# Kernel optimization log

Hardware: AMD Instinct MI355X
Metric: run time of the kernel (lower is better)

## Reference

```python
import jax, jax.numpy as jnp
import numpy as np
from jax import lax

B = 32; L_HIST = 96; FUT = 96; N = 862
D_MODEL = 512; D_STATE = 16; D_CONV = 4; EXPAND = 2
D_INNER = EXPAND * D_MODEL
DT_RANK = (D_MODEL + 15) // 16  # ceil(d_model/16) = 32
D_FF = 512; E_LAYERS = 2; EPS = 1e-5


def setup_inputs() -> dict:
    key = jax.random.key(0)
    ks = iter(jax.random.split(key, 64))
    def rn(shape, scale=0.02):
        return jax.random.normal(next(ks), shape, dtype=jnp.float32) * scale
    f32 = jnp.float32
    inp = {
        "history_data": jax.random.normal(next(ks), (B, L_HIST, N, 1), dtype=f32),
        # RevIN affine
        "revin_w": jnp.ones((N,), f32), "revin_b": jnp.zeros((N,), f32),
        # inverted embedding Linear(L_hist -> d_model)
        "embed_w": rn((D_MODEL, L_HIST)), "embed_b": jnp.zeros((D_MODEL,), f32),
        # Mamba params, stacked over [e_layers, 2 directions]
        "in_proj_w": rn((E_LAYERS, 2, 2 * D_INNER, D_MODEL)),
        "conv_w": rn((E_LAYERS, 2, D_INNER, D_CONV), 0.1),
        "conv_b": jnp.zeros((E_LAYERS, 2, D_INNER), f32),
        "x_proj_w": rn((E_LAYERS, 2, DT_RANK + 2 * D_STATE, D_INNER)),
        "dt_proj_w": rn((E_LAYERS, 2, D_INNER, DT_RANK), 0.1),
        "dt_proj_b": rn((E_LAYERS, 2, D_INNER), 0.1),
        "A_log": jnp.log(jnp.broadcast_to(jnp.arange(1, D_STATE + 1, dtype=f32), (E_LAYERS, 2, D_INNER, D_STATE))),
        "Dp": jnp.ones((E_LAYERS, 2, D_INNER), f32),
        "out_proj_w": rn((E_LAYERS, 2, D_MODEL, D_INNER)),
        # FFN (1x1 conv == linear) + layer norms per layer
        "conv1_w": rn((E_LAYERS, D_FF, D_MODEL)), "conv1_b": jnp.zeros((E_LAYERS, D_FF), f32),
        "conv2_w": rn((E_LAYERS, D_MODEL, D_FF)), "conv2_b": jnp.zeros((E_LAYERS, D_MODEL), f32),
        "norm1_w": jnp.ones((E_LAYERS, D_MODEL), f32), "norm1_b": jnp.zeros((E_LAYERS, D_MODEL), f32),
        "norm2_w": jnp.ones((E_LAYERS, D_MODEL), f32), "norm2_b": jnp.zeros((E_LAYERS, D_MODEL), f32),
        "normf_w": jnp.ones((D_MODEL,), f32), "normf_b": jnp.zeros((D_MODEL,), f32),
        # Projector Linear(d_model -> future_seq_len)
        "proj_w": rn((FUT, D_MODEL)), "proj_b": jnp.zeros((FUT,), f32),
    }
    return inp


def _silu(x):
    return x * jax.nn.sigmoid(x)


def _ln(x, w, b):
    m = x.mean(-1, keepdims=True)
    v = ((x - m) ** 2).mean(-1, keepdims=True)
    return (x - m) / jnp.sqrt(v + EPS) * w + b


def _mamba(x, in_proj_w, conv_w, conv_b, x_proj_w, dt_proj_w, dt_proj_b, A_log, Dp, out_proj_w):
    # x: [B, L, d_model]; L is the channel/token axis here
    xz = jnp.einsum('bld,ed->ble', x, in_proj_w)
    xi, z = jnp.split(xz, 2, axis=-1)  # each [B, L, d_inner]
    # depthwise causal conv1d along L
    xi_t = jnp.pad(jnp.moveaxis(xi, 1, 2), ((0, 0), (0, 0), (D_CONV - 1, 0)))  # [B, di, L+pad]
    conv = lax.conv_general_dilated(xi_t, conv_w[:, None, :], (1,), 'VALID',
                                    feature_group_count=D_INNER)
    xi = _silu(jnp.moveaxis(conv + conv_b[None, :, None], 1, 2))  # [B, L, di]
    # input-dependent dt, B, C
    dbc = jnp.einsum('bld,ed->ble', xi, x_proj_w)
    dt, Bm, Cm = jnp.split(dbc, [DT_RANK, DT_RANK + D_STATE], axis=-1)
    dt = jax.nn.softplus(jnp.einsum('blr,dr->bld', dt, dt_proj_w) + dt_proj_b)  # [B, L, di]
    A = -jnp.exp(A_log)  # [di, n]

    def step(h, inputs):
        dt_t, B_t, C_t, x_t = inputs  # [B,di], [B,n], [B,n], [B,di]
        dA = jnp.exp(dt_t[:, :, None] * A)                       # [B, di, n]
        h = dA * h + (dt_t * x_t)[:, :, None] * B_t[:, None, :]  # [B, di, n]
        y = jnp.einsum('bdn,bn->bd', h, C_t)
        return h, y

    h0 = jnp.zeros((x.shape[0], D_INNER, D_STATE), x.dtype)
    _, ys = lax.scan(step, h0, (dt.swapaxes(0, 1), Bm.swapaxes(0, 1),
                                Cm.swapaxes(0, 1), xi.swapaxes(0, 1)))
    y = ys.swapaxes(0, 1) + xi * Dp  # [B, L, di]
    y = y * _silu(z)
    return jnp.einsum('bld,od->blo', y, out_proj_w)


def reference(history_data, revin_w, revin_b, embed_w, embed_b, in_proj_w, conv_w, conv_b,
              x_proj_w, dt_proj_w, dt_proj_b, A_log, Dp, out_proj_w, conv1_w, conv1_b,
              conv2_w, conv2_b, norm1_w, norm1_b, norm2_w, norm2_b, normf_w, normf_b,
              proj_w, proj_b):
    x = history_data[:, :, :, 0]  # [B, L, N]
    # RevIN norm (stats over time axis, affine per channel)
    mean = x.mean(1, keepdims=True)
    std = jnp.sqrt(x.var(1, keepdims=True) + EPS)
    e = (x - mean) / std * revin_w + revin_b
    # inverted embedding: channels become tokens -> [B, N, d_model]
    e = jnp.einsum('bln,dl->bnd', e, embed_w) + embed_b
    for l in range(E_LAYERS):
        mf = _mamba(e, in_proj_w[l, 0], conv_w[l, 0], conv_b[l, 0], x_proj_w[l, 0],
                    dt_proj_w[l, 0], dt_proj_b[l, 0], A_log[l, 0], Dp[l, 0], out_proj_w[l, 0])
        mr = _mamba(e[:, ::-1, :], in_proj_w[l, 1], conv_w[l, 1], conv_b[l, 1], x_proj_w[l, 1],
                    dt_proj_w[l, 1], dt_proj_b[l, 1], A_log[l, 1], Dp[l, 1], out_proj_w[l, 1])[:, ::-1, :]
        e = _ln(e + mf + mr, norm1_w[l], norm1_b[l])
        y = jnp.maximum(jnp.einsum('bnd,fd->bnf', e, conv1_w[l]) + conv1_b[l], 0.0)  # relu FFN
        y = jnp.einsum('bnf,df->bnd', y, conv2_w[l]) + conv2_b[l]
        e = _ln(e + y, norm2_w[l], norm2_b[l])
    e = _ln(e, normf_w, normf_b)
    dec = jnp.einsum('bnd,fd->bnf', e, proj_w) + proj_b  # [B, N, FUT]
    dec = dec.transpose(0, 2, 1)                          # [B, FUT, N]
    # RevIN denorm
    dec = (dec - revin_b) / (revin_w + EPS * EPS) * std + mean
    return dec[..., None]  # [B, FUT, N, 1]
```

## Files before the change

kernel.cpp:

```cpp
#include <hip/hip_runtime.h>


typedef _Float16 f16;
typedef _Float16 f16x8 __attribute__((ext_vector_type(8)));
typedef _Float16 f16x4 __attribute__((ext_vector_type(4)));
typedef float    f32x4 __attribute__((ext_vector_type(4)));

template<bool B> struct BoolC { static constexpr bool value = B; };

constexpr int Bb  = 32;
constexpr int Lh  = 96;
constexpr int FUTc= 96;
constexpr int Nn  = 862;
constexpr int Dm  = 512;
constexpr int Ds  = 16;
constexpr int Di  = 1024;
constexpr int DRr = 32;
constexpr int TT  = Bb * Nn;
constexpr int NCH = Bb * Di;
constexpr float EPSf = 1e-5f;

__device__ __forceinline__ float sigm(float x){ return 1.f / (1.f + __expf(-x)); }

__device__ __forceinline__ void gll16(f16* lds, const f16* g){
  __builtin_amdgcn_global_load_lds(
      (const __attribute__((address_space(1))) void*)g,
      (__attribute__((address_space(3)))       void*)lds, 16, 0, 0);
}

__global__ __launch_bounds__(256) void stats_kernel(const float* __restrict__ x,
    float* __restrict__ meanb, float* __restrict__ stdb)
{
  int i = blockIdx.x * 256 + threadIdx.x;
  if (i >= TT) return;
  int b = i / Nn, n = i - b * Nn;
  const float* p = x + (size_t)b * Lh * Nn + n;
  float s = 0.f, sq = 0.f;
  #pragma unroll 4
  for (int l = 0; l < Lh; l++){ float v = p[(size_t)l * Nn]; s += v; sq += v * v; }
  float m = s * (1.f / Lh);
  float var = sq * (1.f / Lh) - m * m;
  meanb[i] = m;
  stdb[i]  = sqrtf(var + EPSf);
}

__global__ __launch_bounds__(256) void prep_kernel(const float* __restrict__ x,
    const float* __restrict__ meanb, const float* __restrict__ stdb,
    const float* __restrict__ rw, const float* __restrict__ rb,
    f16* __restrict__ xn16)
{
  int idx = blockIdx.x * 256 + threadIdx.x;
  if (idx >= Bb * Lh * Nn) return;
  int n  = idx % Nn;
  int bl = idx / Nn;
  int l  = bl % Lh;
  int b  = bl / Lh;
  int tok = b * Nn + n;
  float v = x[idx];
  xn16[(size_t)tok * Lh + l] = (f16)((v - meanb[tok]) / stdb[tok] * rw[n] + rb[n]);
}

__global__ __launch_bounds__(256) void cvt_kernel(const float* __restrict__ in,
    f16* __restrict__ out, int n4)
{
  int i = blockIdx.x * 256 + threadIdx.x;
  if (i >= n4) return;
  float4 v = ((const float4*)in)[i];
  f16x4 h; h[0] = (f16)v.x; h[1] = (f16)v.y; h[2] = (f16)v.z; h[3] = (f16)v.w;
  *(f16x4*)(out + (size_t)i * 4) = h;
}

template<int ACT, int ACC, int W32, int W16, int OMIN = 0, int OMAX16 = (1 << 30), int TN = 128>
__global__ __launch_bounds__(256) void gemm16_kernel(
    const f16* __restrict__ A, int lda,
    const f16* __restrict__ W, int K,
    const float* __restrict__ bias,
    float* __restrict__ C, int ldc,
    f16* __restrict__ C16, int ldc16,
    int O, int M)
{
  constexpr int JN = (TN == 64) ? 2 : 4;
  __shared__ f16 As[128 * 32];
  __shared__ f16 Bs[TN * 32];
  const int tid  = threadIdx.x;
  const int lane = tid & 63;
  const int w    = tid >> 6;
  const int wm   = w >> 1, wn = w & 1;
  int bid = blockIdx.y * gridDim.x + blockIdx.x;
  int nwg = gridDim.x * gridDim.y;
  int q = nwg >> 3, r = nwg & 7;
  int xcd = bid & 7, idx = bid >> 3;
  int swz = (xcd < r ? xcd * (q + 1) : r * (q + 1) + (xcd - r) * q) + idx;
  const int m0   = (swz / gridDim.x) * 128, o0 = (swz % gridDim.x) * TN;
  const int wmM  = wm * 64;
  const int wnN  = (TN == 64) ? wn * 32 : wn * 64;
  const int lm   = lane & 15, kg = lane >> 4;
  const int sr0  = w * 32 + (lane >> 2);
  const int sc   = (lane & 3) << 3;

  f32x4 acc[4][JN];
  #pragma unroll
  for (int i = 0; i < 4; i++)
    #pragma unroll
    for (int j = 0; j < JN; j++){ f32x4 z = {0.f,0.f,0.f,0.f}; acc[i][j] = z; }

  for (int k0 = 0; k0 < K; k0 += 32){
    __syncthreads();
    {
      int r0 = min(m0 + sr0,      M - 1);
      int r1 = min(m0 + sr0 + 16, M - 1);
      gll16(&As[w * 1024],       A + (size_t)r0 * lda + k0 + sc);
      gll16(&As[w * 1024 + 512], A + (size_t)r1 * lda + k0 + sc);
      if constexpr (TN == 128){
        int q0 = min(o0 + sr0,      O - 1);
        int q1 = min(o0 + sr0 + 16, O - 1);
        gll16(&Bs[w * 1024],       W + (size_t)q0 * K + k0 + sc);
        gll16(&Bs[w * 1024 + 512], W + (size_t)q1 * K + k0 + sc);
      } else {
        int q0 = min(o0 + w * 16 + (lane >> 2), O - 1);
        gll16(&Bs[w * 512],        W + (size_t)q0 * K + k0 + sc);
      }
    }
    __syncthreads();
    f16x8 af[4], bf[JN];
    #pragma unroll
    for (int f = 0; f < 4; f++)
      af[f] = *(const f16x8*)&As[(wmM + f * 16 + lm) * 32 + kg * 8];
    #pragma unroll
    for (int f = 0; f < JN; f++)
      bf[f] = *(const f16x8*)&Bs[(wnN + f * 16 + lm) * 32 + kg * 8];
    #pragma unroll
    for (int i = 0; i < 4; i++)
      #pragma unroll
      for (int j = 0; j < JN; j++)
        acc[i][j] = __builtin_amdgcn_mfma_f32_16x16x32_f16(af[i], bf[j], acc[i][j], 0, 0, 0);
  }

  f16   pf16[2][4][JN];
  float pf32[2][4][JN];
  auto ldslice = [&](int i, int bank){
    if constexpr (ACT == 3){
      #pragma unroll
      for (int r2 = 0; r2 < 4; r2++){
        int m = min(m0 + wmM + i * 16 + kg * 4 + r2, M - 1);
        #pragma unroll
        for (int j = 0; j < JN; j++){
          int o = min(o0 + wnN + j * 16 + lm, O - 1);
          pf16[bank][r2][j] = C16[(size_t)m * ldc16 + o];
        }
      }
    }
    if constexpr (ACC == 1){
      #pragma unroll
      for (int r2 = 0; r2 < 4; r2++){
        int m = min(m0 + wmM + i * 16 + kg * 4 + r2, M - 1);
        #pragma unroll
        for (int j = 0; j < JN; j++){
          int o = min(o0 + wnN + j * 16 + lm, O - 1);
          if (o >= OMIN) pf32[bank][r2][j] = C[(size_t)m * ldc + (o - OMIN)];
        }
      }
    }
  };
  ldslice(0, 0);
  #pragma unroll
  for (int i = 0; i < 4; i++){
    if (i < 3) ldslice(i + 1, (i + 1) & 1);
    #pragma unroll
    for (int r2 = 0; r2 < 4; r2++){
      int m = m0 + wmM + i * 16 + kg * 4 + r2;
      if (m >= M) continue;
      #pragma unroll
      for (int j = 0; j < JN; j++){
        int o = o0 + wnN + j * 16 + lm;
        if (o >= O) continue;
        float v = acc[i][j][r2];
        if (bias) v += bias[o];
        if (ACT == 1) v = fmaxf(v, 0.f);
        if (ACT == 2) v = fmaxf(v, 0.f) + __logf(1.f + __expf(-fabsf(v)));
        if (ACT == 3){
          float gate = v * sigm(v);
          C16[(size_t)m * ldc16 + o] = (f16)((float)pf16[i & 1][r2][j] * gate);
        } else {
          if (W32 && o >= OMIN){
            if (ACC) v += pf32[i & 1][r2][j];
            C[(size_t)m * ldc + (o - OMIN)] = v;
          }
          if (W16 && o < OMAX16) C16[(size_t)m * ldc16 + o] = (f16)v;
        }
      }
    }
  }
}

template<int DIR>
__global__ __launch_bounds__(256) void conv2_kernel(
    const f16* __restrict__ x16, const float* __restrict__ w,
    const float* __restrict__ cb, f16* __restrict__ xi16)
{
  constexpr int TG = 8;
  constexpr int NG = (Nn + TG - 1) / TG;
  int idx = blockIdx.x * 256 + threadIdx.x;
  if (idx >= Bb * NG * 128) return;
  int d8 = (idx & 127) << 3;
  int gg = idx >> 7;
  int g  = gg % NG, b = gg / NG;
  int n0 = g * TG;
  const f16* base  = x16  + (size_t)b * Nn * 1024 + d8;
  f16*       obase = xi16 + (size_t)b * Nn * 1024 + d8;

  float bias[8];
  {
    float4 c0 = *(const float4*)(cb + d8), c1 = *(const float4*)(cb + d8 + 4);
    bias[0]=c0.x; bias[1]=c0.y; bias[2]=c0.z; bias[3]=c0.w;
    bias[4]=c1.x; bias[5]=c1.y; bias[6]=c1.z; bias[7]=c1.w;
  }
  float wr[4][8];
  #pragma unroll
  for (int i = 0; i < 8; i++){
    float4 wv = *(const float4*)(w + (size_t)(d8 + i) * 4);
    wr[0][i]=wv.x; wr[1][i]=wv.y; wr[2][i]=wv.z; wr[3][i]=wv.w;
  }

  f16x8 zv;
  #pragma unroll
  for (int i = 0; i < 8; i++) zv[i] = (f16)0.f;

  f16x8 win[4];
  #pragma unroll
  for (int j = 0; j < 3; j++){
    int r = DIR ? (n0 + j) : (n0 - 3 + j);
    bool ok = DIR ? (r < Nn) : (r >= 0);
    win[j] = ok ? *(const f16x8*)(base + (size_t)r * 1024) : zv;
  }
  #pragma unroll
  for (int s = 0; s < TG; s++){
    int n = n0 + s;
    if (n < Nn){
      int r = DIR ? (n + 3) : n;
      bool ok = DIR ? (r < Nn) : true;
      win[3] = ok ? *(const f16x8*)(base + (size_t)r * 1024) : zv;
      float acc[8];
      #pragma unroll
      for (int i = 0; i < 8; i++) acc[i] = bias[i];
      #pragma unroll
      for (int k = 0; k < 4; k++){
        const f16x8& rv = DIR ? win[3 - k] : win[k];
        #pragma unroll
        for (int i = 0; i < 8; i++) acc[i] = fmaf(wr[k][i], (float)rv[i], acc[i]);
      }
      f16x8 o;
      #pragma unroll
      for (int i = 0; i < 8; i++){ float a = acc[i]; o[i] = (f16)(a * sigm(a)); }
      *(f16x8*)(obase + (size_t)n * 1024) = o;
      win[0] = win[1]; win[1] = win[2]; win[2] = win[3];
    }
  }
}

__device__ __forceinline__ void pow16(float pp, float* dA){
  float q2 = pp * pp, q3 = q2 * pp, q4 = q2 * q2, q8 = q4 * q4;
  dA[0] = pp;      dA[1] = q2;      dA[2] = q3;      dA[3] = q4;
  dA[4] = q4 * pp; dA[5] = q4 * q2; dA[6] = q4 * q3; dA[7] = q8;
  dA[8] = q8 * pp; dA[9] = q8 * q2; dA[10]= q8 * q3; dA[11]= q8 * q4;
  dA[12]= q8 * dA[4]; dA[13]= q8 * dA[5]; dA[14]= q8 * dA[6]; dA[15]= q8 * q8;
}

template<bool FAST>
__device__ __forceinline__ void mk_dA(float dt, float a0, const float* Aj, float* dA){
  if constexpr (FAST){
    pow16(__expf(dt * a0), dA);
  } else {
    _Pragma("unroll")
    for (int j = 0; j < 16; j++) dA[j] = __expf(dt * Aj[j]);
  }
}

template<int DIR>
__global__ __launch_bounds__(256, 2) void scan_p1_kernel(
    const float* __restrict__ bc, const f16* __restrict__ dt_,
    const f16* __restrict__ xi, const float* __restrict__ A_log,
    float* __restrict__ hseg, float* __restrict__ sdt, int L)
{
  const int seg = blockIdx.y;
  int chain = blockIdx.x * 256 + threadIdx.x;
  int d = chain & 1023;
  int b = __builtin_amdgcn_readfirstlane(chain >> 10);
  float Aj[16];
  #pragma unroll
  for (int q = 0; q < 4; q++){
    float4 al = *(const float4*)(A_log + (size_t)d * 16 + q * 4);
    Aj[q*4+0] = -__expf(al.x); Aj[q*4+1] = -__expf(al.y);
    Aj[q*4+2] = -__expf(al.z); Aj[q*4+3] = -__expf(al.w);
  }
  float a0 = Aj[0];
  int lf = 1;
  #pragma unroll
  for (int j = 1; j < 16; j++)
    lf &= (fabsf(Aj[j] - (j + 1) * a0) <= 2e-3f * (j + 1) * fabsf(a0));
  bool wfast = __all(lf);

  constexpr ptrdiff_t sBC = DIR ? -32 : 32;
  constexpr ptrdiff_t sX  = DIR ? -1024 : 1024;
  int p0 = seg * L;
  size_t tok0 = (size_t)b * Nn + (DIR ? (Nn - 1 - p0) : p0);
  const float* lBC = bc  + tok0 * 32;
  const f16*   lDt = dt_ + tok0 * 1024 + d;
  const f16*   lXi = xi  + tok0 * 1024 + d;

  float h[16];
  #pragma unroll
  for (int j = 0; j < 16; j++) h[j] = 0.f;
  float sacc = 0.f;

  float dtA, xvA, dtB, xvB;
  float4 BA[4], BB[4];

  #define LOADP1(dt_r, xv_r, Bq)                                   \
    { dt_r = (float)*lDt; xv_r = (float)*lXi;                      \
      _Pragma("unroll")                                            \
      for (int q = 0; q < 4; q++) Bq[q] = *(const float4*)(lBC + 4*q); \
      lDt += sX; lXi += sX; lBC += sBC; }

  auto run = [&](auto FAST){
    auto stepv = [&](float dt, float xv, const float4* Bq){
      sacc += dt;
      float dtx = dt * xv;
      float B[16] = {Bq[0].x,Bq[0].y,Bq[0].z,Bq[0].w, Bq[1].x,Bq[1].y,Bq[1].z,Bq[1].w,
                     Bq[2].x,Bq[2].y,Bq[2].z,Bq[2].w, Bq[3].x,Bq[3].y,Bq[3].z,Bq[3].w};
      float dA[16];
      mk_dA<decltype(FAST)::value>(dt, a0, Aj, dA);
      #pragma unroll
      for (int j = 0; j < 16; j++)
        h[j] = fmaf(dA[j], h[j], dtx * B[j]);
    };
    LOADP1(dtA, xvA, BA);
    int t = 0;
    for (; t + 3 <= L; t += 2){
      LOADP1(dtB, xvB, BB);
      asm volatile("" ::: "memory");
      stepv(dtA, xvA, BA);
      LOADP1(dtA, xvA, BA);
      asm volatile("" ::: "memory");
      stepv(dtB, xvB, BB);
    }
    stepv(dtA, xvA, BA); t++;
    if (t < L){ LOADP1(dtB, xvB, BB); stepv(dtB, xvB, BB); }
  };
  if (wfast) run(BoolC<true>{}); else run(BoolC<false>{});
  #undef LOADP1

  float* hp = hseg + ((size_t)seg * NCH + chain) * 16;
  #pragma unroll
  for (int q = 0; q < 4; q++)
    *(float4*)(hp + 4*q) = make_float4(h[q*4], h[q*4+1], h[q*4+2], h[q*4+3]);
  sdt[(size_t)seg * NCH + chain] = sacc;
}

__global__ __launch_bounds__(256) void scan_cb_kernel(
    const float* __restrict__ A_log, float* __restrict__ hseg,
    const float* __restrict__ sdt, int Sm1)
{
  int chain = blockIdx.x * 256 + threadIdx.x;
  int d = chain & 1023;
  float Aj[16];
  #pragma unroll
  for (int q = 0; q < 4; q++){
    float4 al = *(const float4*)(A_log + (size_t)d * 16 + q * 4);
    Aj[q*4+0] = -__expf(al.x); Aj[q*4+1] = -__expf(al.y);
    Aj[q*4+2] = -__expf(al.z); Aj[q*4+3] = -__expf(al.w);
  }
  float tacc[16];
  #pragma unroll
  for (int j = 0; j < 16; j++) tacc[j] = 0.f;
  for (int s = 0; s < Sm1; s++){
    float sd = sdt[(size_t)s * NCH + chain];
    float* hp = hseg + ((size_t)s * NCH + chain) * 16;
    #pragma unroll
    for (int q = 0; q < 4; q++){
      float4 hl = *(const float4*)(hp + 4*q);
      tacc[q*4+0] = fmaf(__expf(Aj[q*4+0] * sd), tacc[q*4+0], hl.x);
      tacc[q*4+1] = fmaf(__expf(Aj[q*4+1] * sd), tacc[q*4+1], hl.y);
      tacc[q*4+2] = fmaf(__expf(Aj[q*4+2] * sd), tacc[q*4+2], hl.z);
      tacc[q*4+3] = fmaf(__expf(Aj[q*4+3] * sd), tacc[q*4+3], hl.w);
      *(float4*)(hp + 4*q) = make_float4(tacc[q*4], tacc[q*4+1], tacc[q*4+2], tacc[q*4+3]);
    }
  }
}

template<int DIR>
__global__ __launch_bounds__(256, 2) void scan_p2_kernel(
    const float* __restrict__ bc, f16* dty, const f16* __restrict__ xi,
    const float* __restrict__ A_log, const float* __restrict__ Dp,
    const float* __restrict__ hseg, int L)
{
  const int seg = blockIdx.y;
  int chain = blockIdx.x * 256 + threadIdx.x;
  int d = chain & 1023;
  int b = __builtin_amdgcn_readfirstlane(chain >> 10);
  float Aj[16];
  #pragma unroll
  for (int q = 0; q < 4; q++){
    float4 al = *(const float4*)(A_log + (size_t)d * 16 + q * 4);
    Aj[q*4+0] = -__expf(al.x); Aj[q*4+1] = -__expf(al.y);
    Aj[q*4+2] = -__expf(al.z); Aj[q*4+3] = -__expf(al.w);
  }
  float a0 = Aj[0];
  int lf = 1;
  #pragma unroll
  for (int j = 1; j < 16; j++)
    lf &= (fabsf(Aj[j] - (j + 1) * a0) <= 2e-3f * (j + 1) * fabsf(a0));
  bool wfast = __all(lf);
  float Dpv = Dp[d];

  constexpr ptrdiff_t sBC = DIR ? -32 : 32;
  constexpr ptrdiff_t sX  = DIR ? -1024 : 1024;
  int p0 = seg * L;
  int len = Nn - p0; if (len > L) len = L;
  size_t tok0 = (size_t)b * Nn + (DIR ? (Nn - 1 - p0) : p0);
  const float* lBC = bc  + tok0 * 32;
  const f16*   lDt = dty + tok0 * 1024 + d;
  const f16*   lXi = xi  + tok0 * 1024 + d;
  f16*         pY  = dty + tok0 * 1024 + d;

  float h[16];
  if (seg){
    const float* hp = hseg + ((size_t)(seg - 1) * NCH + chain) * 16;
    #pragma unroll
    for (int q = 0; q < 4; q++){
      float4 hl = *(const float4*)(hp + 4*q);
      h[q*4+0] = hl.x; h[q*4+1] = hl.y; h[q*4+2] = hl.z; h[q*4+3] = hl.w;
    }
  } else {
    #pragma unroll
    for (int j = 0; j < 16; j++) h[j] = 0.f;
  }

  float dtA, xvA, dtB, xvB;
  float4 QA[8], QB[8];

  #define LOADP2(dt_r, xv_r, Qq)                                   \
    { dt_r = (float)*lDt; xv_r = (float)*lXi;                      \
      _Pragma("unroll")                                            \
      for (int q = 0; q < 8; q++) Qq[q] = *(const float4*)(lBC + 4*q); \
      lDt += sX; lXi += sX; lBC += sBC; }

  auto run = [&](auto FAST){
    auto stepv = [&](float dt, float xv, const float4* Qq){
      float dtx = dt * xv;
      float B[16] = {Qq[0].x,Qq[0].y,Qq[0].z,Qq[0].w, Qq[1].x,Qq[1].y,Qq[1].z,Qq[1].w,
                     Qq[2].x,Qq[2].y,Qq[2].z,Qq[2].w, Qq[3].x,Qq[3].y,Qq[3].z,Qq[3].w};
      float C[16] = {Qq[4].x,Qq[4].y,Qq[4].z,Qq[4].w, Qq[5].x,Qq[5].y,Qq[5].z,Qq[5].w,
                     Qq[6].x,Qq[6].y,Qq[6].z,Qq[6].w, Qq[7].x,Qq[7].y,Qq[7].z,Qq[7].w};
      float dA[16];
      mk_dA<decltype(FAST)::value>(dt, a0, Aj, dA);
      float yv = xv * Dpv;
      #pragma unroll
      for (int j = 0; j < 16; j++){
        h[j] = fmaf(dA[j], h[j], dtx * B[j]);
        yv = fmaf(h[j], C[j], yv);
      }
      *pY = (f16)yv;
      pY += sX;
    };
    LOADP2(dtA, xvA, QA);
    int t = 0;
    for (; t + 3 <= len; t += 2){
      LOADP2(dtB, xvB, QB);
      asm volatile("" ::: "memory");
      stepv(dtA, xvA, QA);
      LOADP2(dtA, xvA, QA);
      asm volatile("" ::: "memory");
      stepv(dtB, xvB, QB);
    }
    stepv(dtA, xvA, QA); t++;
    if (t < len){ LOADP2(dtB, xvB, QB); stepv(dtB, xvB, QB); }
  };
  if (wfast) run(BoolC<true>{}); else run(BoolC<false>{});
  #undef LOADP2
}

__global__ __launch_bounds__(256) void add_ln_kernel(
    float* __restrict__ e, const float* __restrict__ add,
    const float* __restrict__ w, const float* __restrict__ bias,
    f16* __restrict__ e16)
{
  int wv = threadIdx.x >> 6, lane = threadIdx.x & 63;
  int tok = blockIdx.x * 4 + wv;
  float* p = e + (size_t)tok * Dm;
  float4 v0 = ((const float4*)p)[lane * 2];
  float4 v1 = ((const float4*)p)[lane * 2 + 1];
  float x[8] = {v0.x, v0.y, v0.z, v0.w, v1.x, v1.y, v1.z, v1.w};
  if (add){
    const float* q = add + (size_t)tok * Dm;
    float4 a0 = ((const float4*)q)[lane * 2];
    float4 a1 = ((const float4*)q)[lane * 2 + 1];
    x[0] += a0.x; x[1] += a0.y; x[2] += a0.z; x[3] += a0.w;
    x[4] += a1.x; x[5] += a1.y; x[6] += a1.z; x[7] += a1.w;
  }
  float s = 0.f;
  #pragma unroll
  for (int i = 0; i < 8; i++) s += x[i];
  #pragma unroll
  for (int off = 32; off; off >>= 1) s += __shfl_xor(s, off);
  float m = s * (1.f / Dm);
  float vv = 0.f;
  #pragma unroll
  for (int i = 0; i < 8; i++){ float dd = x[i] - m; vv += dd * dd; }
  #pragma unroll
  for (int off = 32; off; off >>= 1) vv += __shfl_xor(vv, off);
  float rs = rsqrtf(vv * (1.f / Dm) + EPSf);
  int db = lane * 8;
  float4 w0 = *(const float4*)(w + db),    w1 = *(const float4*)(w + db + 4);
  float4 b0 = *(const float4*)(bias + db), b1 = *(const float4*)(bias + db + 4);
  float wr[8] = {w0.x, w0.y, w0.z, w0.w, w1.x, w1.y, w1.z, w1.w};
  float br[8] = {b0.x, b0.y, b0.z, b0.w, b1.x, b1.y, b1.z, b1.w};
  float o[8];
  #pragma unroll
  for (int i = 0; i < 8; i++) o[i] = (x[i] - m) * rs * wr[i] + br[i];
  ((float4*)p)[lane * 2]     = make_float4(o[0], o[1], o[2], o[3]);
  ((float4*)p)[lane * 2 + 1] = make_float4(o[4], o[5], o[6], o[7]);
  f16x8 hv;
  #pragma unroll
  for (int i = 0; i < 8; i++) hv[i] = (f16)o[i];
  *(f16x8*)(e16 + (size_t)tok * Dm + db) = hv;
}

__global__ __launch_bounds__(256) void final_kernel(
    const float* __restrict__ dec, const float* __restrict__ meanb,
    const float* __restrict__ stdb, const float* __restrict__ rw,
    const float* __restrict__ rb, float* __restrict__ out)
{
  int idx = blockIdx.x * 256 + threadIdx.x;
  if (idx >= Bb * FUTc * Nn) return;
  int n  = idx % Nn;
  int bf = idx / Nn;
  int f  = bf % FUTc;
  int b  = bf / FUTc;
  int tok = b * Nn + n;
  float v = dec[(size_t)tok * FUTc + f];
  out[idx] = (v - rb[n]) / (rw[n] + 1e-10f) * stdb[tok] + meanb[tok];
}

extern "C" void kernel_launch(void* const* d_in, const int* in_sizes, int n_in,
                              void* d_out, int out_size, void* d_ws, size_t ws_size,
                              hipStream_t stream)
{
  const float* x_hist    = (const float*)d_in[0];
  const float* revin_w   = (const float*)d_in[1];
  const float* revin_b   = (const float*)d_in[2];
  const float* embed_w   = (const float*)d_in[3];
  const float* embed_b   = (const float*)d_in[4];
  const float* in_proj_w = (const float*)d_in[5];
  const float* conv_w    = (const float*)d_in[6];
  const float* conv_b    = (const float*)d_in[7];
  const float* x_proj_w  = (const float*)d_in[8];
  const float* dt_proj_w = (const float*)d_in[9];
  const float* dt_proj_b = (const float*)d_in[10];
  const float* A_log     = (const float*)d_in[11];
  const float* Dp        = (const float*)d_in[12];
  const float* out_proj_w= (const float*)d_in[13];
  const float* conv1_w   = (const float*)d_in[14];
  const float* conv1_b   = (const float*)d_in[15];
  const float* conv2_w   = (const float*)d_in[16];
  const float* conv2_b   = (const float*)d_in[17];
  const float* norm1_w   = (const float*)d_in[18];
  const float* norm1_b   = (const float*)d_in[19];
  const float* norm2_w   = (const float*)d_in[20];
  const float* norm2_b   = (const float*)d_in[21];
  const float* normf_w   = (const float*)d_in[22];
  const float* normf_b   = (const float*)d_in[23];
  const float* proj_w    = (const float*)d_in[24];
  const float* proj_b    = (const float*)d_in[25];

  float* ws    = (float*)d_ws;
  float* meanb = ws;
  float* stdb  = meanb + TT;
  float* e     = stdb + TT;
  f16*   e16   = (f16*)(e + (size_t)TT * Dm);
  f16*   x16   = e16 + (size_t)TT * Dm;
  f16*   xi16  = x16 + (size_t)TT * Di;
  float* bc32  = (float*)(xi16 + (size_t)TT * Di);
  f16*   dt16in= (f16*)(bc32 + (size_t)TT * 32);
  f16*   ipw16 = dt16in + (size_t)TT * 32;
  f16*   opw16 = ipw16 + (size_t)4 * 2048 * Dm;
  f16*   c1w16 = opw16 + (size_t)4 * Dm * Di;
  f16*   c2w16 = c1w16 + (size_t)2 * Dm * Dm;
  f16*   xpw16 = c2w16 + (size_t)2 * Dm * Dm;
  f16*   dtw16 = xpw16 + (size_t)4 * 64 * Di;
  f16*   emw16 = dtw16 + (size_t)4 * Di * DRr;
  f16*   prw16 = emw16 + (size_t)Dm * Lh;
  float* hseg  = (float*)(((uintptr_t)(prw16 + (size_t)FUTc * Dm) + 15) & ~(uintptr_t)15);

  size_t used = (uintptr_t)hseg - (uintptr_t)ws;
  size_t segbytes = ((size_t)NCH * 16 + NCH) * sizeof(float);
  int S = 1;
  if (ws_size > used) S = 1 + (int)((ws_size - used) / segbytes);
  if (S > 8) S = 8;
  if (S < 1) S = 1;
  const int L = (Nn + S - 1) / S;
  float* sdtb = hseg + (size_t)(S > 1 ? S - 1 : 0) * NCH * 16;

  f16*   xn16  = x16;
  f16*   h16   = xi16;
  float* ftmp  = (float*)x16;
  float* dec   = (float*)x16;

  dim3 blk(256);
  auto cvt = [&](const float* in, f16* out, size_t n){
    int n4 = (int)(n / 4);
    cvt_kernel<<<(n4 + 255) / 256, blk, 0, stream>>>(in, out, n4);
  };
  cvt(in_proj_w,  ipw16, (size_t)4 * 2048 * Dm);
  cvt(out_proj_w, opw16, (size_t)4 * Dm * Di);
  cvt(conv1_w,    c1w16, (size_t)2 * Dm * Dm);
  cvt(conv2_w,    c2w16, (size_t)2 * Dm * Dm);
  cvt(x_proj_w,   xpw16, (size_t)4 * 64 * Di);
  cvt(dt_proj_w,  dtw16, (size_t)4 * Di * DRr);
  cvt(embed_w,    emw16, (size_t)Dm * Lh);
  cvt(proj_w,     prw16, (size_t)FUTc * Dm);

  stats_kernel<<<(TT + 255) / 256, blk, 0, stream>>>(x_hist, meanb, stdb);
  prep_kernel<<<(Bb * Lh * Nn + 255) / 256, blk, 0, stream>>>(x_hist, meanb, stdb, revin_w, revin_b, xn16);

  const int gy = (TT + 127) / 128;
  gemm16_kernel<0,0,1,1><<<dim3(4, gy), blk, 0, stream>>>(
      xn16, Lh, emw16, Lh, embed_b, e, Dm, e16, Dm, Dm, TT);

  constexpr int NG = (Nn + 7) / 8;
  const int convGrid = (Bb * NG * 128 + 255) / 256;

  for (int l = 0; l < 2; l++){
    for (int dir = 0; dir < 2; dir++){
      int wi = l * 2 + dir;
      const f16* Wx = ipw16 + (size_t)wi * 2048 * Dm;
      const f16* Wz = Wx + (size_t)Di * Dm;
      const float* Alw = A_log + (size_t)wi * Di * Ds;
      gemm16_kernel<0,0,0,1><<<dim3(8, gy), blk, 0, stream>>>(
          e16, Dm, Wx, Dm, nullptr, nullptr, 0, x16, Di, Di, TT);
      if (dir) conv2_kernel<1><<<convGrid, blk, 0, stream>>>(
                   x16, conv_w + (size_t)wi * Di * 4, conv_b + (size_t)wi * Di, xi16);
      else     conv2_kernel<0><<<convGrid, blk, 0, stream>>>(
                   x16, conv_w + (size_t)wi * Di * 4, conv_b + (size_t)wi * Di, xi16);
      gemm16_kernel<0,0,1,1,32,32,64><<<dim3(1, gy), blk, 0, stream>>>(
          xi16, Di, xpw16 + (size_t)wi * 64 * Di, Di, nullptr,
          bc32, 32, dt16in, 32, 64, TT);
      gemm16_kernel<2,0,0,1><<<dim3(8, gy), blk, 0, stream>>>(
          dt16in, 32, dtw16 + (size_t)wi * Di * DRr, DRr, dt_proj_b + (size_t)wi * Di,
          nullptr, 0, x16, Di, Di, TT);
      if (S > 1){
        if (dir) scan_p1_kernel<1><<<dim3(NCH / 256, S - 1), blk, 0, stream>>>(
                     bc32, x16, xi16, Alw, hseg, sdtb, L);
        else     scan_p1_kernel<0><<<dim3(NCH / 256, S - 1), blk, 0, stream>>>(
                     bc32, x16, xi16, Alw, hseg, sdtb, L);
        scan_cb_kernel<<<NCH / 256, blk, 0, stream>>>(Alw, hseg, sdtb, S - 1);
      }
      if (dir) scan_p2_kernel<1><<<dim3(NCH / 256, S), blk, 0, stream>>>(
                   bc32, x16, xi16, Alw, Dp + (size_t)wi * Di, hseg, L);
      else     scan_p2_kernel<0><<<dim3(NCH / 256, S), blk, 0, stream>>>(
                   bc32, x16, xi16, Alw, Dp + (size_t)wi * Di, hseg, L);
      gemm16_kernel<3,0,0,1><<<dim3(8, gy), blk, 0, stream>>>(
          e16, Dm, Wz, Dm, nullptr, nullptr, 0, x16, Di, Di, TT);
      gemm16_kernel<0,1,1,0><<<dim3(4, gy), blk, 0, stream>>>(
          x16, Di, opw16 + (size_t)wi * Dm * Di, Di, nullptr,
          e, Dm, nullptr, 0, Dm, TT);
    }
    add_ln_kernel<<<TT / 4, blk, 0, stream>>>(e, nullptr, norm1_w + l * Dm, norm1_b + l * Dm, e16);
    gemm16_kernel<1,0,0,1><<<dim3(4, gy), blk, 0, stream>>>(
        e16, Dm, c1w16 + (size_t)l * Dm * Dm, Dm, conv1_b + l * Dm,
        nullptr, 0, h16, Dm, Dm, TT);
    gemm16_kernel<0,0,1,0><<<dim3(4, gy), blk, 0, stream>>>(
        h16, Dm, c2w16 + (size_t)l * Dm * Dm, Dm, conv2_b + l * Dm,
        ftmp, Dm, nullptr, 0, Dm, TT);
    add_ln_kernel<<<TT / 4, blk, 0, stream>>>(e, ftmp, norm2_w + l * Dm, norm2_b + l * Dm, e16);
  }

  add_ln_kernel<<<TT / 4, blk, 0, stream>>>(e, nullptr, normf_w, normf_b, e16);
  gemm16_kernel<0,0,1,0><<<dim3(1, gy), blk, 0, stream>>>(
      e16, Dm, prw16, Dm, proj_b, dec, FUTc, nullptr, 0, FUTc, TT);
  final_kernel<<<(Bb * FUTc * Nn + 255) / 256, blk, 0, stream>>>(
      dec, meanb, stdb, revin_w, revin_b, (float*)d_out);
}
```

Baseline: 2.213 ms.

## Double-buffer GEMM LDS tiles and store fragments in MFMA-native layout

The fp16 GEMM kernel now keeps two LDS buffers per operand and issues the next K-slice's global-to-LDS loads before running the MFMAs on the current slice. This drops one barrier per iteration and is meant to overlap load latency with compute. The LDS layout is also changed so each 16-row fragment is stored contiguously per lane, so fragment reads become linear lane*8 accesses that should avoid bank conflicts. LDS use doubles, which may lower occupancy. Correctness depends on gll16 completion being covered by the single trailing barrier.

Measured after the change: 2.454 ms. 1.11x slower.

```diff
diff --git a/kernel.cpp b/kernel.cpp
--- a/kernel.cpp
+++ b/kernel.cpp
@@ -80,8 +80,8 @@
     int O, int M)
 {
   constexpr int JN = (TN == 64) ? 2 : 4;
-  __shared__ f16 As[128 * 32];
-  __shared__ f16 Bs[TN * 32];
+  __shared__ f16 As[2][128 * 32];
+  __shared__ f16 Bs[2][TN * 32];
   const int tid  = threadIdx.x;
   const int lane = tid & 63;
   const int w    = tid >> 6;
@@ -95,8 +95,7 @@
   const int wmM  = wm * 64;
   const int wnN  = (TN == 64) ? wn * 32 : wn * 64;
   const int lm   = lane & 15, kg = lane >> 4;
-  const int sr0  = w * 32 + (lane >> 2);
-  const int sc   = (lane & 3) << 3;
+  const int lm16 = lane & 15, kch = lane >> 4;
 
   f32x4 acc[4][JN];
   #pragma unroll
@@ -104,36 +103,42 @@
     #pragma unroll
     for (int j = 0; j < JN; j++){ f32x4 z = {0.f,0.f,0.f,0.f}; acc[i][j] = z; }
 
-  for (int k0 = 0; k0 < K; k0 += 32){
-    __syncthreads();
-    {
-      int r0 = min(m0 + sr0,      M - 1);
-      int r1 = min(m0 + sr0 + 16, M - 1);
-      gll16(&As[w * 1024],       A + (size_t)r0 * lda + k0 + sc);
-      gll16(&As[w * 1024 + 512], A + (size_t)r1 * lda + k0 + sc);
-      if constexpr (TN == 128){
-        int q0 = min(o0 + sr0,      O - 1);
-        int q1 = min(o0 + sr0 + 16, O - 1);
-        gll16(&Bs[w * 1024],       W + (size_t)q0 * K + k0 + sc);
-        gll16(&Bs[w * 1024 + 512], W + (size_t)q1 * K + k0 + sc);
-      } else {
-        int q0 = min(o0 + w * 16 + (lane >> 2), O - 1);
-        gll16(&Bs[w * 512],        W + (size_t)q0 * K + k0 + sc);
-      }
-    }
-    __syncthreads();
+  auto stage = [&](int buf, int k0){
+    int fr0 = 2 * w;
+    int r0 = min(m0 + fr0 * 16 + lm16,      M - 1);
+    int r1 = min(m0 + fr0 * 16 + 16 + lm16, M - 1);
+    gll16(&As[buf][(size_t)fr0 * 512],       A + (size_t)r0 * lda + k0 + kch * 8);
+    gll16(&As[buf][(size_t)fr0 * 512 + 512], A + (size_t)r1 * lda + k0 + kch * 8);
+    if constexpr (TN == 128){
+      int q0 = min(o0 + fr0 * 16 + lm16,      O - 1);
+      int q1 = min(o0 + fr0 * 16 + 16 + lm16, O - 1);
+      gll16(&Bs[buf][(size_t)fr0 * 512],       W + (size_t)q0 * K + k0 + kch * 8);
+      gll16(&Bs[buf][(size_t)fr0 * 512 + 512], W + (size_t)q1 * K + k0 + kch * 8);
+    } else {
+      int q0 = min(o0 + w * 16 + lm16, O - 1);
+      gll16(&Bs[buf][(size_t)w * 512], W + (size_t)q0 * K + k0 + kch * 8);
+    }
+  };
+
+  const int NIT = K >> 5;
+  stage(0, 0);
+  __syncthreads();
+  for (int it = 0; it < NIT; ++it){
+    int cur = it & 1;
+    if (it + 1 < NIT) stage(cur ^ 1, (it + 1) << 5);
     f16x8 af[4], bf[JN];
     #pragma unroll
     for (int f = 0; f < 4; f++)
-      af[f] = *(const f16x8*)&As[(wmM + f * 16 + lm) * 32 + kg * 8];
+      af[f] = *(const f16x8*)&As[cur][(size_t)(wm * 4 + f) * 512 + lane * 8];
     #pragma unroll
     for (int f = 0; f < JN; f++)
-      bf[f] = *(const f16x8*)&Bs[(wnN + f * 16 + lm) * 32 + kg * 8];
+      bf[f] = *(const f16x8*)&Bs[cur][(size_t)((TN == 64 ? wn * 2 : wn * 4) + f) * 512 + lane * 8];
     #pragma unroll
     for (int i = 0; i < 4; i++)
       #pragma unroll
       for (int j = 0; j < JN; j++)
         acc[i][j] = __builtin_amdgcn_mfma_f32_16x16x32_f16(af[i], bf[j], acc[i][j], 0, 0, 0);
+    __syncthreads();
   }
 
   f16   pf16[2][4][JN];
```
